# Performance work log

Hardware: AMD Instinct MI355X
Metric: run time of the kernel (lower is better)

## Reference

```python
import jax, jax.numpy as jnp
import numpy as np

N_TOKENS = 100000
UNITS = 150  # CustomizeLSTMCell.TRANSITION_STATE_OUTPUTS_DIM


def setup_inputs() -> dict:
    key = jax.random.key(0)
    ks = jax.random.split(key, 9)
    f = lambda k, shape: jax.random.normal(k, shape, dtype=jnp.float32)
    return {
        "s_in": f(ks[0], (N_TOKENS, UNITS)),
        "s_out": f(ks[1], (N_TOKENS, UNITS)),
        "h_in": f(ks[2], (N_TOKENS, UNITS)),
        "h_out": f(ks[3], (N_TOKENS, UNITS)),
        "last_c": f(ks[4], (N_TOKENS, UNITS)),
        "w_in_input": f(ks[5], (UNITS, UNITS)) * 0.05,
        "w_out_input": f(ks[6], (UNITS, UNITS)) * 0.05,
        "u_in_input": f(ks[7], (UNITS, UNITS)) * 0.05,
        "u_out_input": f(ks[8], (UNITS, UNITS)) * 0.05,
    }


def reference(s_in, s_out, h_in, h_out, last_c,
              w_in_input, w_out_input, u_in_input, u_out_input):
    # Faithful to the source: all four gates use the *_input weights and no bias
    # (the original call() computes identical pre-activations for every gate).
    pre = (s_in @ w_in_input + s_out @ w_out_input
           + h_in @ u_in_input + h_out @ u_out_input)  # [N, H]
    gate = jax.nn.sigmoid(pre)
    # input_gate == output_gate == forget_gate == update_gate == gate
    cell_state = gate * last_c + gate * gate
    hidden_state = gate * jnp.tanh(cell_state)
    return hidden_state, cell_state
```

## Files before the change

kernel.cpp:

```cpp
#include <hip/hip_runtime.h>
#include <hip/hip_bf16.h>

typedef __attribute__((ext_vector_type(8))) short short8;
typedef __attribute__((ext_vector_type(4))) float f32x4;

#define NTOK   100000
#define H      150
#define NKS    20
#define BM     64
#define NCHUNK 38
#define BUFB   (NCHUNK*1024)
#define OUTOFF (NTOK * H)
#define XLIM   ((long)NTOK * H * 4 - 16)

__device__ __forceinline__ unsigned short f2bf(float f) {
    unsigned int u = __builtin_bit_cast(unsigned int, f);
    u = (u + 0x7FFFu + ((u >> 16) & 1u)) >> 16;
    return (unsigned short)u;
}

__global__ void prep_w(const float* __restrict__ w_in, const float* __restrict__ w_out,
                       const float* __restrict__ u_in, const float* __restrict__ u_out,
                       unsigned short* __restrict__ wb) {
    int idx = blockIdx.x * 256 + threadIdx.x;
    if (idx >= 10 * NKS * 64 * 8) return;
    int j    = idx & 7;
    int lane = (idx >> 3) & 63;
    int ks   = (idx >> 9) % NKS;
    int n    = idx / (512 * NKS);
    int seg  = ks / 5, s5 = ks % 5;
    int col  = n * 16 + (lane & 15);
    int k2   = s5 * 32 + (lane >> 4) * 8 + j;
    float v = 0.0f;
    if (col < H && k2 < H) {
        const float* W = (seg == 0) ? w_in : (seg == 1) ? w_out : (seg == 2) ? u_in : u_out;
        v = W[k2 * H + col];
    }
    wb[idx] = f2bf(v);
}

__global__ __launch_bounds__(256, 2) void lstm_fused(
        const float* __restrict__ s_in, const float* __restrict__ s_out,
        const float* __restrict__ h_in, const float* __restrict__ h_out,
        const float* __restrict__ last_c, const unsigned short* __restrict__ wb,
        float* __restrict__ out) {
    __shared__ __align__(16) unsigned char Xr[2][BUFB];

    const int t     = threadIdx.x;
    const int lane  = t & 63;
    const int wid   = t >> 6;
    const int waveM = wid >> 1;
    const int waveN = wid & 1;
    const int lrow  = lane & 15;
    const int lko   = lane >> 4;
    const int r0blk = blockIdx.x * BM;

    const float* Xseg[4] = {s_in, s_out, h_in, h_out};

    f32x4 acc[2][5];
#pragma unroll
    for (int m = 0; m < 2; m++)
#pragma unroll
        for (int n = 0; n < 5; n++) acc[m][n] = (f32x4){0.f, 0.f, 0.f, 0.f};

    auto stage = [&](int seg, int buf) {
        const char* base = (const char*)Xseg[seg];
        const long sofs = (long)r0blk * (H * 4);
#pragma unroll
        for (int i = 0; i < 10; i++) {
            int c = wid + i * 4;
            int cc = (c < NCHUNK) ? c : (c - NCHUNK);
            long go = sofs + cc * 1024 + lane * 16;
            if (go > XLIM) go = XLIM;
            const void* gp = base + go;
            void* lp = &Xr[buf][cc * 1024];
            __builtin_amdgcn_global_load_lds(
                (const __attribute__((address_space(1))) void*)gp,
                (__attribute__((address_space(3))) void*)lp, 16, 0, 0);
        }
    };

    stage(0, 0);
    __syncthreads();

    for (int seg = 0; seg < 4; seg++) {
        short8 bseg[5][5];
#pragma unroll
        for (int s5 = 0; s5 < 5; s5++)
#pragma unroll
            for (int n = 0; n < 5; n++)
                bseg[s5][n] = *(const short8*)
                    &wb[((((long)waveN * 5 + n) * NKS + seg * 5 + s5) * 64 + lane) * 8];

        __builtin_amdgcn_sched_barrier(0);

        if (seg < 3) stage(seg + 1, (seg + 1) & 1);

        __builtin_amdgcn_sched_barrier(0);

        const float* Xf = (const float*)&Xr[seg & 1][0];
#pragma unroll
        for (int s5 = 0; s5 < 5; s5++) {
            const int k0 = s5 * 32 + lko * 8;
            short8 af[2];
#pragma unroll
            for (int m = 0; m < 2; m++) {
                const int row = waveM * 32 + m * 16 + lrow;
                const float* rp = Xf + row * H + k0;
                float xv[8];
#pragma unroll
                for (int j = 0; j < 8; j += 2) {
                    float2 v = *(const float2*)&rp[j];
                    xv[j] = v.x; xv[j + 1] = v.y;
                }
                if (s5 == 4) {
#pragma unroll
                    for (int j = 0; j < 8; j++)
                        xv[j] = (k0 + j < H) ? xv[j] : 0.f;
                }
#pragma unroll
                for (int j = 0; j < 8; j++) af[m][j] = (short)f2bf(xv[j]);
            }
#pragma unroll
            for (int m = 0; m < 2; m++)
#pragma unroll
                for (int n = 0; n < 5; n++)
                    acc[m][n] = __builtin_amdgcn_mfma_f32_16x16x32_bf16(af[m], bseg[s5][n], acc[m][n], 0, 0, 0);
        }
        __syncthreads();
    }

#pragma unroll
    for (int m = 0; m < 2; m++) {
#pragma unroll
        for (int r = 0; r < 4; r++) {
            const int row = r0blk + waveM * 32 + m * 16 + lko * 4 + r;
            if (row >= NTOK) continue;
            const long rb = (long)row * H;
#pragma unroll
            for (int n = 0; n < 5; n++) {
                const int col = waveN * 80 + n * 16 + lrow;
                if (col >= H) continue;
                float pre = acc[m][n][r];
                float e   = __expf(-pre);
                float g   = __builtin_amdgcn_rcpf(1.f + e);
                float lc  = last_c[rb + col];
                float cell = g * lc + g * g;
                float e2  = __expf(-2.f * cell);
                float th  = (1.f - e2) * __builtin_amdgcn_rcpf(1.f + e2);
                out[rb + col]          = g * th;
                out[OUTOFF + rb + col] = cell;
            }
        }
    }
}

extern "C" void kernel_launch(void* const* d_in, const int* in_sizes, int n_in,
                              void* d_out, int out_size, void* d_ws, size_t ws_size,
                              hipStream_t stream) {
    const float* s_in   = (const float*)d_in[0];
    const float* s_out  = (const float*)d_in[1];
    const float* h_in   = (const float*)d_in[2];
    const float* h_out  = (const float*)d_in[3];
    const float* last_c = (const float*)d_in[4];
    const float* w_in   = (const float*)d_in[5];
    const float* w_out  = (const float*)d_in[6];
    const float* u_in   = (const float*)d_in[7];
    const float* u_out  = (const float*)d_in[8];

    unsigned short* wb = (unsigned short*)d_ws;
    float* out = (float*)d_out;

    prep_w<<<(10 * NKS * 64 * 8 + 255) / 256, 256, 0, stream>>>(w_in, w_out, u_in, u_out, wb);

    const int nblocks = (NTOK + BM - 1) / BM;
    lstm_fused<<<nblocks, 256, 0, stream>>>(s_in, s_out, h_in, h_out, last_c, wb, out);
}
```

Before: 128.3 us.

## Split block into eight waves with one M-tile each to raise occupancy

Doubles the workgroup to 512 threads so each wave computes a single 16-row M tile instead of two, halving per-wave accumulator and A-fragment registers. Staging loads are spread over eight waves. The aim is more resident waves to hide global and LDS latency in a memory-bound fused GEMM. In exchange, each wave reloads the full weight fragments, doubling B-fragment traffic per block.

```diff
diff --git a/kernel.cpp b/kernel.cpp
--- a/kernel.cpp
+++ b/kernel.cpp
@@ -39,7 +39,7 @@
     wb[idx] = f2bf(v);
 }
 
-__global__ __launch_bounds__(256, 2) void lstm_fused(
+__global__ __launch_bounds__(512, 4) void lstm_fused(
         const float* __restrict__ s_in, const float* __restrict__ s_out,
         const float* __restrict__ h_in, const float* __restrict__ h_out,
         const float* __restrict__ last_c, const unsigned short* __restrict__ wb,
@@ -57,23 +57,18 @@
 
     const float* Xseg[4] = {s_in, s_out, h_in, h_out};
 
-    f32x4 acc[2][5];
+    f32x4 acc[5];
 #pragma unroll
-    for (int m = 0; m < 2; m++)
-#pragma unroll
-        for (int n = 0; n < 5; n++) acc[m][n] = (f32x4){0.f, 0.f, 0.f, 0.f};
+    for (int n = 0; n < 5; n++) acc[n] = (f32x4){0.f, 0.f, 0.f, 0.f};
 
     auto stage = [&](int seg, int buf) {
         const char* base = (const char*)Xseg[seg];
         const long sofs = (long)r0blk * (H * 4);
-#pragma unroll
-        for (int i = 0; i < 10; i++) {
-            int c = wid + i * 4;
-            int cc = (c < NCHUNK) ? c : (c - NCHUNK);
-            long go = sofs + cc * 1024 + lane * 16;
+        for (int c = wid; c < NCHUNK; c += 8) {
+            long go = sofs + c * 1024 + lane * 16;
             if (go > XLIM) go = XLIM;
             const void* gp = base + go;
-            void* lp = &Xr[buf][cc * 1024];
+            void* lp = &Xr[buf][c * 1024];
             __builtin_amdgcn_global_load_lds(
                 (const __attribute__((address_space(1))) void*)gp,
                 (__attribute__((address_space(3))) void*)lp, 16, 0, 0);
@@ -99,58 +94,50 @@
         __builtin_amdgcn_sched_barrier(0);
 
         const float* Xf = (const float*)&Xr[seg & 1][0];
+        const int row = waveM * 16 + lrow;
 #pragma unroll
         for (int s5 = 0; s5 < 5; s5++) {
             const int k0 = s5 * 32 + lko * 8;
-            short8 af[2];
+            const float* rp = Xf + row * H + k0;
+            float xv[8];
 #pragma unroll
-            for (int m = 0; m < 2; m++) {
-                const int row = waveM * 32 + m * 16 + lrow;
-                const float* rp = Xf + row * H + k0;
-                float xv[8];
+            for (int j = 0; j < 8; j += 2) {
+                float2 v = *(const float2*)&rp[j];
+                xv[j] = v.x; xv[j + 1] = v.y;
+            }
+            if (s5 == 4) {
 #pragma unroll
-                for (int j = 0; j < 8; j += 2) {
-                    float2 v = *(const float2*)&rp[j];
-                    xv[j] = v.x; xv[j + 1] = v.y;
-                }
-                if (s5 == 4) {
+                for (int j = 0; j < 8; j++)
+                    xv[j] = (k0 + j < H) ? xv[j] : 0.f;
+            }
+            short8 af;
 #pragma unroll
-                    for (int j = 0; j < 8; j++)
-                        xv[j] = (k0 + j < H) ? xv[j] : 0.f;
-                }
+            for (int j = 0; j < 8; j++) af[j] = (short)f2bf(xv[j]);
 #pragma unroll
-                for (int j = 0; j < 8; j++) af[m][j] = (short)f2bf(xv[j]);
-            }
-#pragma unroll
-            for (int m = 0; m < 2; m++)
-#pragma unroll
-                for (int n = 0; n < 5; n++)
-                    acc[m][n] = __builtin_amdgcn_mfma_f32_16x16x32_bf16(af[m], bseg[s5][n], acc[m][n], 0, 0, 0);
+            for (int n = 0; n < 5; n++)
+                acc[n] = __builtin_amdgcn_mfma_f32_16x16x32_bf16(af, bseg[s5][n], acc[n], 0, 0, 0);
         }
         __syncthreads();
     }
 
 #pragma unroll
-    for (int m = 0; m < 2; m++) {
+    for (int r = 0; r < 4; r++) {
+        const int row = r0blk + waveM * 16 + lko * 4 + r;
+        if (row >= NTOK) continue;
+        const long rb = (long)row * H;
 #pragma unroll
-        for (int r = 0; r < 4; r++) {
-            const int row = r0blk + waveM * 32 + m * 16 + lko * 4 + r;
-            if (row >= NTOK) continue;
-            const long rb = (long)row * H;
-#pragma unroll
-            for (int n = 0; n < 5; n++) {
-                const int col = waveN * 80 + n * 16 + lrow;
-                if (col >= H) continue;
-                float pre = acc[m][n][r];
-                float e   = __expf(-pre);
-                float g   = __builtin_amdgcn_rcpf(1.f + e);
-                float lc  = last_c[rb + col];
-                float cell = g * lc + g * g;
-                float e2  = __expf(-2.f * cell);
-                float th  = (1.f - e2) * __builtin_amdgcn_rcpf(1.f + e2);
-                out[rb + col]          = g * th;
-                out[OUTOFF + rb + col] = cell;
-            }
+        for (int n = 0; n < 5; n++) {
+            const int col = waveN * 80 + n * 16 + lrow;
+            if (col >= H) continue;
+            float pre = acc[n][r];
+            float e   = __expf(-pre);
+            float g   = __builtin_amdgcn_rcpf(1.f + e);
+            float lc  = last_c[rb + col];
+            float cell = g * lc + g * g;
+            float e2  = __expf(-2.f * cell);
+            float th  = (1.f - e2) * __builtin_amdgcn_rcpf(1.f + e2);
+            out[rb + col]          = g * th;
+            out[OUTOFF + rb + col] = cell;
         }
     }
 }
@@ -174,5 +161,5 @@
     prep_w<<<(10 * NKS * 64 * 8 + 255) / 256, 256, 0, stream>>>(w_in, w_out, u_in, u_out, wb);
 
     const int nblocks = (NTOK + BM - 1) / BM;
-    lstm_fused<<<nblocks, 256, 0, stream>>>(s_in, s_out, h_in, h_out, last_c, wb, out);
+    lstm_fused<<<nblocks, 512, 0, stream>>>(s_in, s_out, h_in, h_out, last_c, wb, out);
 }
```

New measurement: 172.1 us. 1.34x slower.
